# Kernel optimization log

Hardware: AMD Instinct MI355X
Metric: run time of the kernel (lower is better)

The kernel has to match this reference:

```python
import jax, jax.numpy as jnp
import numpy as np

EMBED_DIM = 584
HEADS = 8
HEAD_SIZE = EMBED_DIM // HEADS  # 73
CTX = 200


def setup_inputs() -> dict:
    key = jax.random.key(0)
    ks = jax.random.split(key, 6)
    B, T = 256, 200
    x = jax.random.normal(ks[0], (B, T, EMBED_DIM), dtype=jnp.float32)
    s = 1.0 / np.sqrt(EMBED_DIM)
    # per-head q/k/v Linear(EMBED_DIM, HEAD_SIZE, bias=False) weights, stacked: [H, hs, E]
    Wq = jax.random.uniform(ks[1], (HEADS, HEAD_SIZE, EMBED_DIM), jnp.float32, -s, s)
    Wk = jax.random.uniform(ks[2], (HEADS, HEAD_SIZE, EMBED_DIM), jnp.float32, -s, s)
    Wv = jax.random.uniform(ks[3], (HEADS, HEAD_SIZE, EMBED_DIM), jnp.float32, -s, s)
    Wo = jax.random.uniform(ks[4], (EMBED_DIM, EMBED_DIM), jnp.float32, -s, s)
    bo = jax.random.uniform(ks[5], (EMBED_DIM,), jnp.float32, -s, s)
    return {"x": x, "Wq": Wq, "Wk": Wk, "Wv": Wv, "Wo": Wo, "bo": bo}


def reference(x, Wq, Wk, Wv, Wo, bo):
    B, T, C = x.shape  # C == EMBED_DIM
    # per-head projections, batched: [B, H, T, hs]
    q = jnp.einsum('bte,hfe->bhtf', x, Wq)
    k = jnp.einsum('bte,hfe->bhtf', x, Wk)
    v = jnp.einsum('bte,hfe->bhtf', x, Wv)
    # NOTE: original scales by EMBED_DIM**-0.5 (C), not head_size**-0.5
    scores = jnp.einsum('bhtf,bhsf->bhts', q, k) * (C ** -0.5)
    causal = jnp.tril(jnp.ones((T, T), dtype=bool))
    scores = jnp.where(causal, scores, -jnp.inf)
    w = jax.nn.softmax(scores, axis=-1)
    out = jnp.einsum('bhts,bhsf->bhtf', w, v)  # [B,H,T,hs]
    out = out.transpose(0, 2, 1, 3).reshape(B, T, C)  # concat heads on last dim
    return out @ Wo.T + bo
```

## Files before the change

kernel.cpp:

```cpp
#include <hip/hip_runtime.h>

typedef __bf16 bf16x8 __attribute__((ext_vector_type(8)));
typedef __bf16 bf16x4 __attribute__((ext_vector_type(4)));
typedef float f32x4 __attribute__((ext_vector_type(4)));

#define EMBED 584
#define KP 608
#define HEADS 8
#define HS 73
#define HSQ 80
#define CTX 200
#define NBATCH 256
#define MROWS 51200
#define NQKV 1752

#define CH 112
#define KSS 104
#define VTS 136
#define PSS 136

__device__ __forceinline__ void gld_lds16(__bf16* lds, const __bf16* g) {
  __builtin_amdgcn_global_load_lds(
      (const __attribute__((address_space(1))) void*)g,
      (__attribute__((address_space(3))) void*)lds, 16, 0, 0);
}

__global__ __launch_bounds__(256) void cvt_x(const float* __restrict__ x,
                                             __bf16* __restrict__ out) {
  int i = blockIdx.x * 256 + threadIdx.x;
  int r = i / 76, slot = i - r * 76;
  int col = slot * 8;
  bf16x8 o8 = {};
  if (col < EMBED) {
    const float4* s4 = (const float4*)(x + (size_t)r * EMBED + col);
    float4 f0 = s4[0], f1 = s4[1];
    o8[0] = (__bf16)f0.x; o8[1] = (__bf16)f0.y; o8[2] = (__bf16)f0.z; o8[3] = (__bf16)f0.w;
    o8[4] = (__bf16)f1.x; o8[5] = (__bf16)f1.y; o8[6] = (__bf16)f1.z; o8[7] = (__bf16)f1.w;
  }
  *(bf16x8*)(out + (size_t)r * KP + col) = o8;
}

__global__ __launch_bounds__(256) void pack_w(const float* __restrict__ Wq,
                                              const float* __restrict__ Wk,
                                              const float* __restrict__ Wv,
                                              const float* __restrict__ Wo,
                                              __bf16* __restrict__ out) {
  int i = blockIdx.x * 256 + threadIdx.x;
  if (i >= 2336 * 76) return;
  int r = i / 76, slot = i - r * 76;
  int col = slot * 8;
  bf16x8 o8 = {};
  if (col < EMBED) {
    const float* src = r < 584  ? Wq + (size_t)r * EMBED
                     : r < 1168 ? Wk + (size_t)(r - 584) * EMBED
                     : r < 1752 ? Wv + (size_t)(r - 1168) * EMBED
                                : Wo + (size_t)(r - 1752) * EMBED;
    const float4* s4 = (const float4*)(src + col);
    float4 f0 = s4[0], f1 = s4[1];
    o8[0] = (__bf16)f0.x; o8[1] = (__bf16)f0.y; o8[2] = (__bf16)f0.z; o8[3] = (__bf16)f0.w;
    o8[4] = (__bf16)f1.x; o8[5] = (__bf16)f1.y; o8[6] = (__bf16)f1.z; o8[7] = (__bf16)f1.w;
  }
  *(bf16x8*)(out + (size_t)r * KP + col) = o8;
}

__global__ __launch_bounds__(256) void gemm_qkv(const __bf16* __restrict__ A,
                                                const __bf16* __restrict__ Bm,
                                                __bf16* __restrict__ Q,
                                                __bf16* __restrict__ Ko,
                                                __bf16* __restrict__ V) {
  constexpr int N = NQKV;
  __shared__ __bf16 As[128 * 32];
  __shared__ __bf16 Bs[128 * 32];
  int tid = threadIdx.x;
  int bn = blockIdx.x, bm = blockIdx.y;
  int wid = tid >> 6, lane = tid & 63;
  int wm = (wid & 1) * 64, wn = (wid >> 1) * 64;
  int lr = lane & 15, lq = lane >> 4;
  const __bf16* aB = A  + (size_t)(bm * 128 + wid * 32 + (lane >> 2)) * KP + (lane & 3) * 8;
  const __bf16* bB = Bm + (size_t)(bn * 128 + wid * 32 + (lane >> 2)) * KP + (lane & 3) * 8;
  __bf16* asD = As + wid * 1024;
  __bf16* bsD = Bs + wid * 1024;
  f32x4 acc[4][4] = {};
  for (int kt = 0; kt < 19; ++kt) {
    int k0 = kt * 32;
    gld_lds16(asD,       aB + k0);
    gld_lds16(asD + 512, aB + 16 * KP + k0);
    gld_lds16(bsD,       bB + k0);
    gld_lds16(bsD + 512, bB + 16 * KP + k0);
    __syncthreads();
    bf16x8 af[4], bfr[4];
#pragma unroll
    for (int i = 0; i < 4; ++i)
      af[i] = *(const bf16x8*)&As[(wm + i * 16 + lr) * 32 + lq * 8];
#pragma unroll
    for (int j = 0; j < 4; ++j)
      bfr[j] = *(const bf16x8*)&Bs[(wn + j * 16 + lr) * 32 + lq * 8];
#pragma unroll
    for (int i = 0; i < 4; ++i)
#pragma unroll
      for (int j = 0; j < 4; ++j)
        acc[i][j] = __builtin_amdgcn_mfma_f32_16x16x32_bf16(af[i], bfr[j], acc[i][j], 0, 0, 0);
    __syncthreads();
  }
#pragma unroll
  for (int i = 0; i < 4; ++i) {
    int m = bm * 128 + wm + i * 16 + lq * 4;
#pragma unroll
    for (int j = 0; j < 4; ++j) {
      int n = bn * 128 + wn + j * 16 + lr;
      if (n < N) {
        int which = n / EMBED;
        int rem = n - which * EMBED;
        int hh = rem / HS;
        int f = rem - hh * HS;
#pragma unroll
        for (int r = 0; r < 4; ++r) {
          int mm = m + r;
          int bb = mm / CTX;
          int tt = mm - bb * CTX;
          int bh = bb * HEADS + hh;
          __bf16 val = (__bf16)acc[i][j][r];
          if (which == 0)
            Q[((size_t)bh * CTX + tt) * HSQ + f] = val;
          else if (which == 1)
            Ko[((size_t)bh * CTX + tt) * HSQ + f] = val;
          else
            V[((size_t)bh * HSQ + f) * CTX + tt] = val;
        }
      }
    }
  }
}

__global__ __launch_bounds__(256) void attn_kernel(const __bf16* __restrict__ q,
                                                   const __bf16* __restrict__ k,
                                                   const __bf16* __restrict__ v,
                                                   __bf16* __restrict__ o) {
  __shared__ __align__(16) __bf16 lds[31232];
  __bf16* Ks = lds;
  __bf16* Vt = lds + 11648;
  __bf16* Ps = lds + 22528;

  int tid = threadIdx.x;
  int bh = blockIdx.x;
  int b = bh >> 3, h = bh & 7;
  const __bf16* qg = q + (size_t)bh * (CTX * HSQ);
  const __bf16* kg = k + (size_t)bh * (CTX * HSQ);
  const __bf16* vg = v + (size_t)bh * (HSQ * CTX);

  {
    f32x4* p = (f32x4*)lds;
    for (int i = tid; i < 3904; i += 256) p[i] = f32x4{0.f, 0.f, 0.f, 0.f};
  }
  if (h == 0) {
    bf16x8 z = {};
    for (int i = tid; i < CTX * 3; i += 256) {
      int t = i / 3, seg = i - t * 3;
      *(bf16x8*)&o[((size_t)(b * CTX + t)) * KP + EMBED + seg * 8] = z;
    }
  }
  __syncthreads();

  int wid = tid >> 6, lane = tid & 63;
  int lr = lane & 15, g = lane >> 4;
  __bf16* Pw = Ps + wid * (16 * PSS);
  const int nstr = (wid == 0) ? 4 : 3;
  const float scale = 0.04138029443264672f;

  float ml[4][4], ll[4][4];
  f32x4 ov[4][5];
#pragma unroll
  for (int i = 0; i < 4; ++i)
#pragma unroll
    for (int r = 0; r < 4; ++r) { ml[i][r] = -1e30f; ll[i][r] = 0.f; }
#pragma unroll
  for (int i = 0; i < 4; ++i)
#pragma unroll
    for (int nt = 0; nt < 5; ++nt) ov[i][nt] = f32x4{0.f, 0.f, 0.f, 0.f};

  for (int c = 0; c < 2; ++c) {
    int key0 = c * CH;
    for (int idx = tid; idx < CH * 10; idx += 256) {
      int s = idx / 10, slot = idx % 10;
      int key = key0 + s;
      if (key < CTX)
        *(bf16x8*)&Ks[s * KSS + slot * 8] =
            *(const bf16x8*)&kg[(size_t)key * HSQ + slot * 8];
    }
    for (int idx = tid; idx < HSQ * 14; idx += 256) {
      int f = idx / 14, slot = idx % 14;
      int s0 = slot * 8;
      bf16x8 vv;
      if (key0 + s0 + 7 < CTX) {
        vv = *(const bf16x8*)&vg[(size_t)f * CTX + key0 + s0];
      } else {
#pragma unroll
        for (int j = 0; j < 8; ++j)
          vv[j] = (key0 + s0 + j < CTX) ? vg[(size_t)f * CTX + key0 + s0 + j]
                                        : (__bf16)0.f;
      }
      *(bf16x8*)&Vt[f * VTS + s0] = vv;
    }
    __syncthreads();

#pragma unroll
    for (int i = 0; i < 4; ++i) {
      if (i >= nstr) break;
      int strip = wid + 4 * i;
      int row0 = strip * 16;
      bf16x8 qf[3];
      qf[0] = *(const bf16x8*)&qg[(size_t)(row0 + lr) * HSQ + g * 8];
      qf[1] = *(const bf16x8*)&qg[(size_t)(row0 + lr) * HSQ + 32 + g * 8];
      if (g < 2)
        qf[2] = *(const bf16x8*)&qg[(size_t)(row0 + lr) * HSQ + 64 + g * 8];
      else
        qf[2] = bf16x8{};
      float sc[7][4];
#pragma unroll
      for (int nt = 0; nt < 7; ++nt) {
        f32x4 acc = {};
#pragma unroll
        for (int kc = 0; kc < 3; ++kc) {
          bf16x8 kf = *(const bf16x8*)&Ks[(nt * 16 + lr) * KSS + kc * 32 + g * 8];
          acc = __builtin_amdgcn_mfma_f32_16x16x32_bf16(qf[kc], kf, acc, 0, 0, 0);
        }
        int kcol = key0 + nt * 16 + lr;
#pragma unroll
        for (int r = 0; r < 4; ++r) {
          int qrow = row0 + g * 4 + r;
          sc[nt][r] = (kcol <= qrow && kcol < CTX) ? acc[r] * scale : -1e30f;
        }
      }
      float mc[4];
#pragma unroll
      for (int r = 0; r < 4; ++r) {
        float m = sc[0][r];
#pragma unroll
        for (int nt = 1; nt < 7; ++nt) m = fmaxf(m, sc[nt][r]);
        mc[r] = m;
      }
#pragma unroll
      for (int off = 8; off; off >>= 1)
#pragma unroll
        for (int r = 0; r < 4; ++r)
          mc[r] = fmaxf(mc[r], __shfl_xor(mc[r], off, 64));
      float alpha[4], rs[4];
#pragma unroll
      for (int r = 0; r < 4; ++r) {
        float mnew = fmaxf(ml[i][r], mc[r]);
        alpha[r] = __expf(ml[i][r] - mnew);
        ml[i][r] = mnew;
        float s = 0.f;
#pragma unroll
        for (int nt = 0; nt < 7; ++nt) {
          sc[nt][r] = __expf(sc[nt][r] - mnew);
          s += sc[nt][r];
        }
        rs[r] = s;
      }
#pragma unroll
      for (int off = 8; off; off >>= 1)
#pragma unroll
        for (int r = 0; r < 4; ++r) rs[r] += __shfl_xor(rs[r], off, 64);
#pragma unroll
      for (int r = 0; r < 4; ++r) ll[i][r] = ll[i][r] * alpha[r] + rs[r];
#pragma unroll
      for (int nt = 0; nt < 5; ++nt)
#pragma unroll
        for (int r = 0; r < 4; ++r) ov[i][nt][r] *= alpha[r];
#pragma unroll
      for (int nt = 0; nt < 7; ++nt)
#pragma unroll
        for (int r = 0; r < 4; ++r)
          Pw[(g * 4 + r) * PSS + nt * 16 + lr] = (__bf16)sc[nt][r];
#pragma unroll
      for (int kc = 0; kc < 4; ++kc) {
        bf16x8 pf = *(const bf16x8*)&Pw[lr * PSS + kc * 32 + g * 8];
#pragma unroll
        for (int nt = 0; nt < 5; ++nt) {
          bf16x8 vf = *(const bf16x8*)&Vt[(nt * 16 + lr) * VTS + kc * 32 + g * 8];
          ov[i][nt] = __builtin_amdgcn_mfma_f32_16x16x32_bf16(pf, vf, ov[i][nt], 0, 0, 0);
        }
      }
    }
    __syncthreads();
  }
#pragma unroll
  for (int i = 0; i < 4; ++i) {
    if (i >= nstr) break;
    int strip = wid + 4 * i;
    float inv[4];
#pragma unroll
    for (int r = 0; r < 4; ++r) inv[r] = 1.0f / ll[i][r];
#pragma unroll
    for (int nt = 0; nt < 5; ++nt) {
      int f = nt * 16 + lr;
      if (f < HS) {
#pragma unroll
        for (int r = 0; r < 4; ++r) {
          int t = strip * 16 + g * 4 + r;
          if (t < CTX)
            o[((size_t)(b * CTX + t)) * KP + h * HS + f] =
                (__bf16)(ov[i][nt][r] * inv[r]);
        }
      }
    }
  }
}

__global__ __launch_bounds__(256) void gemm_out(const __bf16* __restrict__ A,
                                                const __bf16* __restrict__ Bm,
                                                const float* __restrict__ bias,
                                                float* __restrict__ C) {
  constexpr int N = EMBED;
  __shared__ __bf16 As[128 * 32];
  __shared__ __bf16 Bs[128 * 32];
  int tid = threadIdx.x;
  int bn = blockIdx.x, bm = blockIdx.y;
  int wid = tid >> 6, lane = tid & 63;
  int wm = (wid & 1) * 64, wn = (wid >> 1) * 64;
  int lr = lane & 15, lq = lane >> 4;
  const __bf16* aB = A  + (size_t)(bm * 128 + wid * 32 + (lane >> 2)) * KP + (lane & 3) * 8;
  const __bf16* bB = Bm + (size_t)(bn * 128 + wid * 32 + (lane >> 2)) * KP + (lane & 3) * 8;
  __bf16* asD = As + wid * 1024;
  __bf16* bsD = Bs + wid * 1024;
  f32x4 acc[4][4] = {};
  for (int kt = 0; kt < 19; ++kt) {
    int k0 = kt * 32;
    gld_lds16(asD,       aB + k0);
    gld_lds16(asD + 512, aB + 16 * KP + k0);
    gld_lds16(bsD,       bB + k0);
    gld_lds16(bsD + 512, bB + 16 * KP + k0);
    __syncthreads();
    bf16x8 af[4], bfr[4];
#pragma unroll
    for (int i = 0; i < 4; ++i)
      af[i] = *(const bf16x8*)&As[(wm + i * 16 + lr) * 32 + lq * 8];
#pragma unroll
    for (int j = 0; j < 4; ++j)
      bfr[j] = *(const bf16x8*)&Bs[(wn + j * 16 + lr) * 32 + lq * 8];
#pragma unroll
    for (int i = 0; i < 4; ++i)
#pragma unroll
      for (int j = 0; j < 4; ++j)
        acc[i][j] = __builtin_amdgcn_mfma_f32_16x16x32_bf16(af[i], bfr[j], acc[i][j], 0, 0, 0);
    __syncthreads();
  }
#pragma unroll
  for (int i = 0; i < 4; ++i) {
    int m = bm * 128 + wm + i * 16 + lq * 4;
#pragma unroll
    for (int j = 0; j < 4; ++j) {
      int n = bn * 128 + wn + j * 16 + lr;
      if (n < N) {
        float bval = bias[n];
#pragma unroll
        for (int r = 0; r < 4; ++r)
          C[(size_t)(m + r) * N + n] = acc[i][j][r] + bval;
      }
    }
  }
}

extern "C" void kernel_launch(void* const* d_in, const int* in_sizes, int n_in,
                              void* d_out, int out_size, void* d_ws, size_t ws_size,
                              hipStream_t stream) {
  const float* x  = (const float*)d_in[0];
  const float* Wq = (const float*)d_in[1];
  const float* Wk = (const float*)d_in[2];
  const float* Wv = (const float*)d_in[3];
  const float* Wo = (const float*)d_in[4];
  const float* bo = (const float*)d_in[5];
  float* out = (float*)d_out;

  __bf16* xb   = (__bf16*)d_ws;
  __bf16* wcat = xb + 31129600ULL;
  __bf16* qb   = wcat + 1420288ULL;
  __bf16* kb   = qb + 32768000ULL;
  __bf16* vb   = kb + 32768000ULL;
  __bf16* ab   = xb;

  cvt_x<<<15200, 256, 0, stream>>>(x, xb);
  pack_w<<<694, 256, 0, stream>>>(Wq, Wk, Wv, Wo, wcat);
  gemm_qkv<<<dim3(14, 400), 256, 0, stream>>>(xb, wcat, qb, kb, vb);
  attn_kernel<<<2048, 256, 0, stream>>>(qb, kb, vb, ab);
  gemm_out<<<dim3(5, 400), 256, 0, stream>>>(ab, wcat + 1752ULL * KP, bo, out);
}
```

Baseline: 745.3 us.

## Double-buffer GEMM LDS tiles, swizzle block ids, vectorize QKV epilogue stores

Both the QKV and output-projection GEMMs now use two LDS buffers. The next K-tile's global-to-LDS load is issued before the current tile's MFMAs, and there is one barrier per iteration instead of two, so load latency can overlap with compute. Block indices are remapped to a 1D grid with an interleaved (id&7) permutation, meant to improve L2 locality across the chip's partitions. The QKV epilogue hoists the per-column head and offset math out of the row loop and writes V transposed as packed 4-element bf16 stores. In exchange, LDS use per block doubles, which may reduce occupancy.

```diff
diff --git a/kernel.cpp b/kernel.cpp
--- a/kernel.cpp
+++ b/kernel.cpp
@@ -68,65 +68,83 @@
                                                 __bf16* __restrict__ Q,
                                                 __bf16* __restrict__ Ko,
                                                 __bf16* __restrict__ V) {
-  constexpr int N = NQKV;
-  __shared__ __bf16 As[128 * 32];
-  __shared__ __bf16 Bs[128 * 32];
+  __shared__ __bf16 As[2][4096];
+  __shared__ __bf16 Bs[2][4096];
   int tid = threadIdx.x;
-  int bn = blockIdx.x, bm = blockIdx.y;
+  int id = blockIdx.x;
+  int idp = (id & 7) * 700 + (id >> 3);
+  int bm = idp / 14, bn = idp - bm * 14;
   int wid = tid >> 6, lane = tid & 63;
   int wm = (wid & 1) * 64, wn = (wid >> 1) * 64;
   int lr = lane & 15, lq = lane >> 4;
   const __bf16* aB = A  + (size_t)(bm * 128 + wid * 32 + (lane >> 2)) * KP + (lane & 3) * 8;
   const __bf16* bB = Bm + (size_t)(bn * 128 + wid * 32 + (lane >> 2)) * KP + (lane & 3) * 8;
-  __bf16* asD = As + wid * 1024;
-  __bf16* bsD = Bs + wid * 1024;
   f32x4 acc[4][4] = {};
+  gld_lds16(As[0] + wid * 1024,       aB);
+  gld_lds16(As[0] + wid * 1024 + 512, aB + 16 * KP);
+  gld_lds16(Bs[0] + wid * 1024,       bB);
+  gld_lds16(Bs[0] + wid * 1024 + 512, bB + 16 * KP);
+  __syncthreads();
+  int cur = 0;
   for (int kt = 0; kt < 19; ++kt) {
-    int k0 = kt * 32;
-    gld_lds16(asD,       aB + k0);
-    gld_lds16(asD + 512, aB + 16 * KP + k0);
-    gld_lds16(bsD,       bB + k0);
-    gld_lds16(bsD + 512, bB + 16 * KP + k0);
-    __syncthreads();
+    if (kt < 18) {
+      int k0 = (kt + 1) * 32;
+      gld_lds16(As[cur ^ 1] + wid * 1024,       aB + k0);
+      gld_lds16(As[cur ^ 1] + wid * 1024 + 512, aB + 16 * KP + k0);
+      gld_lds16(Bs[cur ^ 1] + wid * 1024,       bB + k0);
+      gld_lds16(Bs[cur ^ 1] + wid * 1024 + 512, bB + 16 * KP + k0);
+    }
     bf16x8 af[4], bfr[4];
 #pragma unroll
     for (int i = 0; i < 4; ++i)
-      af[i] = *(const bf16x8*)&As[(wm + i * 16 + lr) * 32 + lq * 8];
+      af[i] = *(const bf16x8*)&As[cur][(wm + i * 16 + lr) * 32 + lq * 8];
 #pragma unroll
     for (int j = 0; j < 4; ++j)
-      bfr[j] = *(const bf16x8*)&Bs[(wn + j * 16 + lr) * 32 + lq * 8];
+      bfr[j] = *(const bf16x8*)&Bs[cur][(wn + j * 16 + lr) * 32 + lq * 8];
 #pragma unroll
     for (int i = 0; i < 4; ++i)
 #pragma unroll
       for (int j = 0; j < 4; ++j)
         acc[i][j] = __builtin_amdgcn_mfma_f32_16x16x32_bf16(af[i], bfr[j], acc[i][j], 0, 0, 0);
-    __syncthreads();
+    if (kt < 18) __syncthreads();
+    cur ^= 1;
+  }
+  int whichj[4], ojv[4];
+  __bf16* Pj[4];
+  bool okj[4];
+#pragma unroll
+  for (int j = 0; j < 4; ++j) {
+    int n = bn * 128 + wn + j * 16 + lr;
+    okj[j] = (n < NQKV);
+    int nn = okj[j] ? n : 0;
+    int which = nn / EMBED;
+    int rem = nn - which * EMBED;
+    int hh = rem / HS;
+    int f = rem - hh * HS;
+    whichj[j] = which;
+    ojv[j] = (which == 2) ? (hh * 16000 + f * 200) : (hh * 16000 + f);
+    Pj[j] = (which == 0) ? Q : (which == 1) ? Ko : V;
   }
 #pragma unroll
   for (int i = 0; i < 4; ++i) {
-    int m = bm * 128 + wm + i * 16 + lq * 4;
+    int m0 = bm * 128 + wm + i * 16 + lq * 4;
+    int bb = m0 / CTX;
+    int tt = m0 - bb * CTX;
+    int a_qk = bb * 128000 + tt * 80;
+    int a_v  = bb * 128000 + tt;
 #pragma unroll
     for (int j = 0; j < 4; ++j) {
-      int n = bn * 128 + wn + j * 16 + lr;
-      if (n < N) {
-        int which = n / EMBED;
-        int rem = n - which * EMBED;
-        int hh = rem / HS;
-        int f = rem - hh * HS;
-#pragma unroll
-        for (int r = 0; r < 4; ++r) {
-          int mm = m + r;
-          int bb = mm / CTX;
-          int tt = mm - bb * CTX;
-          int bh = bb * HEADS + hh;
-          __bf16 val = (__bf16)acc[i][j][r];
-          if (which == 0)
-            Q[((size_t)bh * CTX + tt) * HSQ + f] = val;
-          else if (which == 1)
-            Ko[((size_t)bh * CTX + tt) * HSQ + f] = val;
-          else
-            V[((size_t)bh * HSQ + f) * CTX + tt] = val;
-        }
+      if (!okj[j]) continue;
+      if (whichj[j] == 2) {
+        bf16x4 v4;
+#pragma unroll
+        for (int r = 0; r < 4; ++r) v4[r] = (__bf16)acc[i][j][r];
+        *(bf16x4*)&Pj[j][a_v + ojv[j]] = v4;
+      } else {
+        int base = a_qk + ojv[j];
+#pragma unroll
+        for (int r = 0; r < 4; ++r)
+          Pj[j][base + r * 80] = (__bf16)acc[i][j][r];
       }
     }
   }
@@ -313,38 +331,46 @@
                                                 const float* __restrict__ bias,
                                                 float* __restrict__ C) {
   constexpr int N = EMBED;
-  __shared__ __bf16 As[128 * 32];
-  __shared__ __bf16 Bs[128 * 32];
+  __shared__ __bf16 As[2][4096];
+  __shared__ __bf16 Bs[2][4096];
   int tid = threadIdx.x;
-  int bn = blockIdx.x, bm = blockIdx.y;
+  int id = blockIdx.x;
+  int idp = (id & 7) * 250 + (id >> 3);
+  int bm = idp / 5, bn = idp - bm * 5;
   int wid = tid >> 6, lane = tid & 63;
   int wm = (wid & 1) * 64, wn = (wid >> 1) * 64;
   int lr = lane & 15, lq = lane >> 4;
   const __bf16* aB = A  + (size_t)(bm * 128 + wid * 32 + (lane >> 2)) * KP + (lane & 3) * 8;
   const __bf16* bB = Bm + (size_t)(bn * 128 + wid * 32 + (lane >> 2)) * KP + (lane & 3) * 8;
-  __bf16* asD = As + wid * 1024;
-  __bf16* bsD = Bs + wid * 1024;
   f32x4 acc[4][4] = {};
+  gld_lds16(As[0] + wid * 1024,       aB);
+  gld_lds16(As[0] + wid * 1024 + 512, aB + 16 * KP);
+  gld_lds16(Bs[0] + wid * 1024,       bB);
+  gld_lds16(Bs[0] + wid * 1024 + 512, bB + 16 * KP);
+  __syncthreads();
+  int cur = 0;
   for (int kt = 0; kt < 19; ++kt) {
-    int k0 = kt * 32;
-    gld_lds16(asD,       aB + k0);
-    gld_lds16(asD + 512, aB + 16 * KP + k0);
-    gld_lds16(bsD,       bB + k0);
-    gld_lds16(bsD + 512, bB + 16 * KP + k0);
-    __syncthreads();
+    if (kt < 18) {
+      int k0 = (kt + 1) * 32;
+      gld_lds16(As[cur ^ 1] + wid * 1024,       aB + k0);
+      gld_lds16(As[cur ^ 1] + wid * 1024 + 512, aB + 16 * KP + k0);
+      gld_lds16(Bs[cur ^ 1] + wid * 1024,       bB + k0);
+      gld_lds16(Bs[cur ^ 1] + wid * 1024 + 512, bB + 16 * KP + k0);
+    }
     bf16x8 af[4], bfr[4];
 #pragma unroll
     for (int i = 0; i < 4; ++i)
-      af[i] = *(const bf16x8*)&As[(wm + i * 16 + lr) * 32 + lq * 8];
+      af[i] = *(const bf16x8*)&As[cur][(wm + i * 16 + lr) * 32 + lq * 8];
 #pragma unroll
     for (int j = 0; j < 4; ++j)
-      bfr[j] = *(const bf16x8*)&Bs[(wn + j * 16 + lr) * 32 + lq * 8];
+      bfr[j] = *(const bf16x8*)&Bs[cur][(wn + j * 16 + lr) * 32 + lq * 8];
 #pragma unroll
     for (int i = 0; i < 4; ++i)
 #pragma unroll
       for (int j = 0; j < 4; ++j)
         acc[i][j] = __builtin_amdgcn_mfma_f32_16x16x32_bf16(af[i], bfr[j], acc[i][j], 0, 0, 0);
-    __syncthreads();
+    if (kt < 18) __syncthreads();
+    cur ^= 1;
   }
 #pragma unroll
   for (int i = 0; i < 4; ++i) {
@@ -382,7 +408,7 @@
 
   cvt_x<<<15200, 256, 0, stream>>>(x, xb);
   pack_w<<<694, 256, 0, stream>>>(Wq, Wk, Wv, Wo, wcat);
-  gemm_qkv<<<dim3(14, 400), 256, 0, stream>>>(xb, wcat, qb, kb, vb);
+  gemm_qkv<<<5600, 256, 0, stream>>>(xb, wcat, qb, kb, vb);
   attn_kernel<<<2048, 256, 0, stream>>>(qb, kb, vb, ab);
-  gemm_out<<<dim3(5, 400), 256, 0, stream>>>(ab, wcat + 1752ULL * KP, bo, out);
-}
+  gemm_out<<<2000, 256, 0, stream>>>(ab, wcat + 1752ULL * KP, bo, out);
+}
```

Measured after the change: 728.7 us. 2.2% less time.
